# Kernel tuning notes

Hardware: AMD Instinct MI355X
Metric: run time of the kernel (lower is better)

Reference implementation:

```python
import jax, jax.numpy as jnp
from jax import lax
import numpy as np

HIDDEN = 64
B, T = 256, 3000


def setup_inputs() -> dict:
    key = jax.random.key(0)
    ks = jax.random.split(key, 7)
    s = 1.0 / np.sqrt(HIDDEN)  # torch default uniform(-1/sqrt(H), 1/sqrt(H))
    u = lambda k, shape: jax.random.uniform(k, shape, jnp.float32, -s, s)
    return {
        "x": jax.random.normal(ks[0], (B, T, 1), dtype=jnp.float32),
        "W_ih": u(ks[1], (3 * HIDDEN, 1)),
        "W_hh": u(ks[2], (3 * HIDDEN, HIDDEN)),
        "b_ih": u(ks[3], (3 * HIDDEN,)),
        "b_hh": u(ks[4], (3 * HIDDEN,)),
        "W_fc": u(ks[5], (1, HIDDEN)),
        "b_fc": u(ks[6], (1,)),
    }


def reference(x, W_ih, W_hh, b_ih, b_hh, W_fc, b_fc):
    # Precompute input contributions to all three gates for all timesteps: (B, T, 3H)
    gi = jnp.einsum("bti,gi->btg", x, W_ih) + b_ih

    def step(h, gi_t):
        gh = h @ W_hh.T + b_hh                      # (B, 3H)
        i_r, i_z, i_n = jnp.split(gi_t, 3, axis=-1)  # torch gate order: r, z, n
        h_r, h_z, h_n = jnp.split(gh, 3, axis=-1)
        r = jax.nn.sigmoid(i_r + h_r)
        z = jax.nn.sigmoid(i_z + h_z)
        n = jnp.tanh(i_n + r * h_n)
        h_new = (1.0 - z) * n + z * h
        return h_new, None

    h0 = jnp.zeros((x.shape[0], HIDDEN), dtype=x.dtype)
    hT, _ = lax.scan(step, h0, jnp.swapaxes(gi, 0, 1))  # scan over T
    # fc(o[:, -1]).squeeze() -> (B,)
    return (hT @ W_fc.T + b_fc).squeeze(-1)
```

## Files before the change

### kernel.cpp

```cpp
#include <hip/hip_runtime.h>
#include <math.h>

#define T_LEN 3000
#define HID 64

typedef _Float16 f16;
typedef f16 f16x8 __attribute__((ext_vector_type(8)));
typedef float f32x4 __attribute__((ext_vector_type(4)));

__device__ __forceinline__ float sigmoid_f(float v) {
    return __builtin_amdgcn_rcpf(1.0f + __expf(-v));
}
__device__ __forceinline__ float tanh_f(float v) {
    return fmaf(2.0f, __builtin_amdgcn_rcpf(1.0f + __expf(-2.0f * v)), -1.0f);
}

__global__ __launch_bounds__(256, 1)
void gru_4wave(
    const float* __restrict__ x,
    const float* __restrict__ W_ih,
    const float* __restrict__ W_hh,
    const float* __restrict__ b_ih,
    const float* __restrict__ b_hh,
    const float* __restrict__ W_fc,
    const float* __restrict__ b_fc,
    float* __restrict__ out)
{
    const int tid = threadIdx.x;
    const int w   = tid >> 6;
    const int l   = tid & 63;
    const int col = l & 15;
    const int grp = l >> 4;
    const int b   = blockIdx.x;
    const int u   = 16 * w + col;
    const long xbase = (long)b * T_LEN;

    __shared__ __align__(16) f16 hbuf[2][HID];
    __shared__ float hf32[HID];

    f16x8 Bf[3][2];
#pragma unroll
    for (int g = 0; g < 3; ++g) {
#pragma unroll
        for (int hf = 0; hf < 2; ++hf) {
            const float* p = W_hh + (size_t)(64 * g + 16 * w + col) * HID
                           + 8 * grp + 32 * hf;
            const float4 a = *reinterpret_cast<const float4*>(p);
            const float4 c = *reinterpret_cast<const float4*>(p + 4);
            f16x8 v;
            v[0] = (f16)a.x; v[1] = (f16)a.y; v[2] = (f16)a.z; v[3] = (f16)a.w;
            v[4] = (f16)c.x; v[5] = (f16)c.y; v[6] = (f16)c.z; v[7] = (f16)c.w;
            Bf[g][hf] = v;
        }
    }

    const float wihr = W_ih[u],        wihz = W_ih[64 + u],   wihn = W_ih[128 + u];
    const float br   = b_ih[u]        + b_hh[u];
    const float bz   = b_ih[64 + u]   + b_hh[64 + u];
    const float bin  = b_ih[128 + u];
    const float bhn  = b_hh[128 + u];

    float xwin = x[xbase + l];
    float xnxt = (64 + l < T_LEN) ? x[xbase + 64 + l] : 0.0f;

    if (tid < HID) hbuf[0][tid] = (f16)0.0f;
    __syncthreads();

    float h = 0.0f;
    const f32x4 zf = {0.f, 0.f, 0.f, 0.f};

    auto step = [&](const f16* hsrc_raw, f16* hdst, int t) {
        const int j = t & 63;
        const float xt = __builtin_bit_cast(
            float, __builtin_amdgcn_readlane(__builtin_bit_cast(int, xwin), j));
        const float gxr = fmaf(xt, wihr, br);
        const float gxz = fmaf(xt, wihz, bz);
        const float gxn = fmaf(xt, wihn, bin);

        const f16x8* hsrc = reinterpret_cast<const f16x8*>(hsrc_raw);
        const f16x8 A0 = hsrc[grp];
        const f16x8 A1 = hsrc[grp + 4];

        f32x4 c0r = __builtin_amdgcn_mfma_f32_16x16x32_f16(A0, Bf[0][0], zf, 0, 0, 0);
        f32x4 c0z = __builtin_amdgcn_mfma_f32_16x16x32_f16(A0, Bf[1][0], zf, 0, 0, 0);
        f32x4 c0n = __builtin_amdgcn_mfma_f32_16x16x32_f16(A0, Bf[2][0], zf, 0, 0, 0);
        f32x4 ccr = __builtin_amdgcn_mfma_f32_16x16x32_f16(A1, Bf[0][1], c0r, 0, 0, 0);
        f32x4 ccz = __builtin_amdgcn_mfma_f32_16x16x32_f16(A1, Bf[1][1], c0z, 0, 0, 0);
        f32x4 ccn = __builtin_amdgcn_mfma_f32_16x16x32_f16(A1, Bf[2][1], c0n, 0, 0, 0);

        const float r = sigmoid_f(gxr + ccr[0]);
        const float z = sigmoid_f(gxz + ccz[0]);
        const float n = tanh_f(fmaf(r, ccn[0] + bhn, gxn));
        h = fmaf(z, h - n, n);

        if (grp == 0) hdst[u] = (f16)h;
        if (j == 63) {
            xwin = xnxt;
            const int idx = t + 65 + l;
            xnxt = (idx < T_LEN) ? x[xbase + idx] : 0.0f;
        }
        __syncthreads();
    };

    for (int t = 0; t < T_LEN; t += 2) {
        step(hbuf[0], hbuf[1], t);
        step(hbuf[1], hbuf[0], t + 1);
    }

    if (grp == 0) hf32[u] = h;
    __syncthreads();
    if (tid < HID) {
        float v = hf32[tid] * W_fc[tid];
#pragma unroll
        for (int off = 32; off > 0; off >>= 1) v += __shfl_down(v, off);
        if (tid == 0) out[b] = v + b_fc[0];
    }
}

extern "C" void kernel_launch(void* const* d_in, const int* in_sizes, int n_in,
                              void* d_out, int out_size, void* d_ws, size_t ws_size,
                              hipStream_t stream) {
    const float* x    = (const float*)d_in[0];
    const float* W_ih = (const float*)d_in[1];
    const float* W_hh = (const float*)d_in[2];
    const float* b_ih = (const float*)d_in[3];
    const float* b_hh = (const float*)d_in[4];
    const float* W_fc = (const float*)d_in[5];
    const float* b_fc = (const float*)d_in[6];
    float* out = (float*)d_out;

    const int B = 256;
    gru_4wave<<<B, 256, 0, stream>>>(x, W_ih, W_hh, b_ih, b_hh, W_fc, b_fc, out);
}
```

Measured before the change: 645.5 us.

## Process two batch sequences per workgroup to interleave independent GRU chains

```diff
diff --git a/kernel.cpp b/kernel.cpp
--- a/kernel.cpp
+++ b/kernel.cpp
@@ -14,9 +14,13 @@
 __device__ __forceinline__ float tanh_f(float v) {
     return fmaf(2.0f, __builtin_amdgcn_rcpf(1.0f + __expf(-2.0f * v)), -1.0f);
 }
+__device__ __forceinline__ float bcast_lane(float v, int j) {
+    return __builtin_bit_cast(float,
+        __builtin_amdgcn_readlane(__builtin_bit_cast(int, v), j));
+}
 
 __global__ __launch_bounds__(256, 1)
-void gru_4wave(
+void gru_2batch(
     const float* __restrict__ x,
     const float* __restrict__ W_ih,
     const float* __restrict__ W_hh,
@@ -31,12 +35,13 @@
     const int l   = tid & 63;
     const int col = l & 15;
     const int grp = l >> 4;
-    const int b   = blockIdx.x;
     const int u   = 16 * w + col;
-    const long xbase = (long)b * T_LEN;
+    const int b0  = 2 * blockIdx.x;
+    const long xb0 = (long)b0 * T_LEN;
+    const long xb1 = xb0 + T_LEN;
 
-    __shared__ __align__(16) f16 hbuf[2][HID];
-    __shared__ float hf32[HID];
+    __shared__ __align__(16) f16 hbuf[2][2][HID];
+    __shared__ float hf32[2][HID];
 
     f16x8 Bf[3][2];
 #pragma unroll
@@ -60,46 +65,66 @@
     const float bin  = b_ih[128 + u];
     const float bhn  = b_hh[128 + u];
 
-    float xwin = x[xbase + l];
-    float xnxt = (64 + l < T_LEN) ? x[xbase + 64 + l] : 0.0f;
+    float xw0 = x[xb0 + l];
+    float xw1 = x[xb1 + l];
+    float xn0 = (64 + l < T_LEN) ? x[xb0 + 64 + l] : 0.0f;
+    float xn1 = (64 + l < T_LEN) ? x[xb1 + 64 + l] : 0.0f;
 
-    if (tid < HID) hbuf[0][tid] = (f16)0.0f;
+    if (tid < 2 * HID) reinterpret_cast<f16*>(hbuf[0])[tid] = (f16)0.0f;
     __syncthreads();
 
-    float h = 0.0f;
+    float h0 = 0.0f, h1 = 0.0f;
     const f32x4 zf = {0.f, 0.f, 0.f, 0.f};
 
-    auto step = [&](const f16* hsrc_raw, f16* hdst, int t) {
+    auto step = [&](const f16(*src)[HID], f16(*dst)[HID], int t) {
         const int j = t & 63;
-        const float xt = __builtin_bit_cast(
-            float, __builtin_amdgcn_readlane(__builtin_bit_cast(int, xwin), j));
-        const float gxr = fmaf(xt, wihr, br);
-        const float gxz = fmaf(xt, wihz, bz);
-        const float gxn = fmaf(xt, wihn, bin);
+        const float xt0 = bcast_lane(xw0, j);
+        const float xt1 = bcast_lane(xw1, j);
+        const float gxr0 = fmaf(xt0, wihr, br);
+        const float gxz0 = fmaf(xt0, wihz, bz);
+        const float gxn0 = fmaf(xt0, wihn, bin);
+        const float gxr1 = fmaf(xt1, wihr, br);
+        const float gxz1 = fmaf(xt1, wihz, bz);
+        const float gxn1 = fmaf(xt1, wihn, bin);
 
-        const f16x8* hsrc = reinterpret_cast<const f16x8*>(hsrc_raw);
-        const f16x8 A0 = hsrc[grp];
-        const f16x8 A1 = hsrc[grp + 4];
+        const f16x8* h0v = reinterpret_cast<const f16x8*>(src[0]);
+        const f16x8* h1v = reinterpret_cast<const f16x8*>(src[1]);
+        const f16x8 A00 = h0v[grp], A01 = h0v[grp + 4];
+        const f16x8 A10 = h1v[grp], A11 = h1v[grp + 4];
 
-        f32x4 c0r = __builtin_amdgcn_mfma_f32_16x16x32_f16(A0, Bf[0][0], zf, 0, 0, 0);
-        f32x4 c0z = __builtin_amdgcn_mfma_f32_16x16x32_f16(A0, Bf[1][0], zf, 0, 0, 0);
-        f32x4 c0n = __builtin_amdgcn_mfma_f32_16x16x32_f16(A0, Bf[2][0], zf, 0, 0, 0);
-        f32x4 ccr = __builtin_amdgcn_mfma_f32_16x16x32_f16(A1, Bf[0][1], c0r, 0, 0, 0);
-        f32x4 ccz = __builtin_amdgcn_mfma_f32_16x16x32_f16(A1, Bf[1][1], c0z, 0, 0, 0);
-        f32x4 ccn = __builtin_amdgcn_mfma_f32_16x16x32_f16(A1, Bf[2][1], c0n, 0, 0, 0);
+        f32x4 p0r = __builtin_amdgcn_mfma_f32_16x16x32_f16(A00, Bf[0][0], zf, 0, 0, 0);
+        f32x4 p0z = __builtin_amdgcn_mfma_f32_16x16x32_f16(A00, Bf[1][0], zf, 0, 0, 0);
+        f32x4 p0n = __builtin_amdgcn_mfma_f32_16x16x32_f16(A00, Bf[2][0], zf, 0, 0, 0);
+        f32x4 p1r = __builtin_amdgcn_mfma_f32_16x16x32_f16(A10, Bf[0][0], zf, 0, 0, 0);
+        f32x4 p1z = __builtin_amdgcn_mfma_f32_16x16x32_f16(A10, Bf[1][0], zf, 0, 0, 0);
+        f32x4 p1n = __builtin_amdgcn_mfma_f32_16x16x32_f16(A10, Bf[2][0], zf, 0, 0, 0);
+        f32x4 q0r = __builtin_amdgcn_mfma_f32_16x16x32_f16(A01, Bf[0][1], p0r, 0, 0, 0);
+        f32x4 q0z = __builtin_amdgcn_mfma_f32_16x16x32_f16(A01, Bf[1][1], p0z, 0, 0, 0);
+        f32x4 q0n = __builtin_amdgcn_mfma_f32_16x16x32_f16(A01, Bf[2][1], p0n, 0, 0, 0);
+        f32x4 q1r = __builtin_amdgcn_mfma_f32_16x16x32_f16(A11, Bf[0][1], p1r, 0, 0, 0);
+        f32x4 q1z = __builtin_amdgcn_mfma_f32_16x16x32_f16(A11, Bf[1][1], p1z, 0, 0, 0);
+        f32x4 q1n = __builtin_amdgcn_mfma_f32_16x16x32_f16(A11, Bf[2][1], p1n, 0, 0, 0);
 
-        const float r = sigmoid_f(gxr + ccr[0]);
-        const float z = sigmoid_f(gxz + ccz[0]);
-        const float n = tanh_f(fmaf(r, ccn[0] + bhn, gxn));
-        h = fmaf(z, h - n, n);
+        const float r0 = sigmoid_f(gxr0 + q0r[0]);
+        const float r1 = sigmoid_f(gxr1 + q1r[0]);
+        const float z0 = sigmoid_f(gxz0 + q0z[0]);
+        const float z1 = sigmoid_f(gxz1 + q1z[0]);
+        const float n0 = tanh_f(fmaf(r0, q0n[0] + bhn, gxn0));
+        const float n1 = tanh_f(fmaf(r1, q1n[0] + bhn, gxn1));
+        h0 = fmaf(z0, h0 - n0, n0);
+        h1 = fmaf(z1, h1 - n1, n1);
 
-        if (grp == 0) hdst[u] = (f16)h;
+        if (grp == 0) {
+            dst[0][u] = (f16)h0;
+            dst[1][u] = (f16)h1;
+        }
         if (j == 63) {
-            xwin = xnxt;
+            xw0 = xn0; xw1 = xn1;
             const int idx = t + 65 + l;
-            xnxt = (idx < T_LEN) ? x[xbase + idx] : 0.0f;
+            xn0 = (idx < T_LEN) ? x[xb0 + idx] : 0.0f;
+            xn1 = (idx < T_LEN) ? x[xb1 + idx] : 0.0f;
         }
-        __syncthreads();
+        asm volatile("s_waitcnt lgkmcnt(0)\n\ts_barrier" ::: "memory");
     };
 
     for (int t = 0; t < T_LEN; t += 2) {
@@ -107,13 +132,15 @@
         step(hbuf[1], hbuf[0], t + 1);
     }
 
-    if (grp == 0) hf32[u] = h;
+    if (grp == 0) { hf32[0][u] = h0; hf32[1][u] = h1; }
     __syncthreads();
-    if (tid < HID) {
-        float v = hf32[tid] * W_fc[tid];
+    if (tid < 2 * HID) {
+        const int e = tid >> 6;
+        const int i = tid & 63;
+        float v = hf32[e][i] * W_fc[i];
 #pragma unroll
         for (int off = 32; off > 0; off >>= 1) v += __shfl_down(v, off);
-        if (tid == 0) out[b] = v + b_fc[0];
+        if (i == 0) out[b0 + e] = v + b_fc[0];
     }
 }
 
@@ -130,5 +157,5 @@
     float* out = (float*)d_out;
 
     const int B = 256;
-    gru_4wave<<<B, 256, 0, stream>>>(x, W_ih, W_hh, b_ih, b_hh, W_fc, b_fc, out);
+    gru_2batch<<<B / 2, 256, 0, stream>>>(x, W_ih, W_hh, b_ih, b_hh, W_fc, b_fc, out);
 }
```

Result: slower. 946.0 us (+46.6%).
